# Kernel tuning notes

Hardware: AMD Instinct MI355X
Metric: run time of the kernel (lower is better)

Reference implementation:

```python
import jax, jax.numpy as jnp
import numpy as np

D_MODEL = 1024
N_HEADS = 16
D_HEAD = D_MODEL // N_HEADS
EPS_LN = 1e-5
EPS_GATE = 1e-5
EPS_DEN = 1e-5


def setup_inputs() -> dict:
    key = jax.random.key(0)
    ks = jax.random.split(key, 4)
    B, T, D = 1, 2048, D_MODEL
    x = jax.random.normal(ks[0], (B, T, D), dtype=jnp.float32)
    # Linear weights scaled like torch default init (~1/sqrt(fan_in))
    s = 1.0 / np.sqrt(D)
    qkv_w = jax.random.normal(ks[1], (3 * D, D), dtype=jnp.float32) * s
    gate_w = jax.random.normal(ks[2], (D, D), dtype=jnp.float32) * s
    proj_w = jax.random.normal(ks[3], (D, D), dtype=jnp.float32) * s
    return {
        "x": x,
        "ln_g": jnp.ones((D,), jnp.float32),
        "ln_b": jnp.zeros((D,), jnp.float32),
        "qkv_w": qkv_w,
        "qkv_b": jnp.zeros((3 * D,), jnp.float32),
        "gate_w": gate_w,
        "gate_b": jnp.zeros((D,), jnp.float32),
        "proj_w": proj_w,
        "proj_b": jnp.zeros((D,), jnp.float32),
    }


def _linear(x, w, b):
    # torch nn.Linear: y = x @ W^T + b, W is (out, in)
    return jnp.einsum("btd,od->bto", x, w) + b


def reference(x, ln_g, ln_b, qkv_w, qkv_b, gate_w, gate_b, proj_w, proj_b):
    B, T, D = x.shape
    H, Dh = N_HEADS, D_HEAD

    # LayerNorm
    mu = jnp.mean(x, axis=-1, keepdims=True)
    var = jnp.mean((x - mu) ** 2, axis=-1, keepdims=True)
    x_norm = (x - mu) / jnp.sqrt(var + EPS_LN) * ln_g + ln_b

    qkv = _linear(x_norm, qkv_w, qkv_b)
    q, k, v = jnp.split(qkv, 3, axis=-1)

    # concept gate on raw x
    gate_sig = jax.nn.sigmoid(_linear(x, gate_w, gate_b))
    gate_norm = gate_sig / (jnp.mean(gate_sig, axis=-1, keepdims=True) + EPS_GATE)
    q = q * gate_norm
    k = k * gate_norm

    # (B,T,D) -> (B,H,T,Dh)
    def heads(t):
        return t.reshape(B, T, H, Dh).transpose(0, 2, 1, 3)

    q, k, v = heads(q).astype(jnp.float32), heads(k).astype(jnp.float32), heads(v).astype(jnp.float32)

    q = jax.nn.elu(q) + 1.0
    k = jax.nn.elu(k) + 1.0

    # causal linear attention via cumsum of outer products (same math as source)
    kv = jnp.einsum("bhtd,bhtm->bhtdm", k, v)        # (B,H,T,Dh,Dh)
    kv_cum = jnp.cumsum(kv, axis=2)
    out_num = jnp.einsum("bhtd,bhtdm->bhtm", q, kv_cum)
    k_cum = jnp.cumsum(k, axis=2)
    out_den = jnp.einsum("bhtd,bhtd->bht", q, k_cum)[..., None] + EPS_DEN
    out = out_num / out_den                           # (B,H,T,Dh)

    out = out.astype(x_norm.dtype).transpose(0, 2, 1, 3).reshape(B, T, D)
    return _linear(out, proj_w, proj_b)
```

## Files before the change

kernel.cpp:

```cpp
#include <hip/hip_runtime.h>
#include <hip/hip_bf16.h>
#include <math.h>

#define T_SEQ 2048
#define DM 1024
#define NH 16
#define DH 64
#define CHUNK 64
#define NCHUNK (T_SEQ / CHUNK)

typedef __hip_bfloat16 bf16;
typedef __attribute__((ext_vector_type(8))) short short8;
typedef __attribute__((ext_vector_type(4))) short short4v;
typedef __attribute__((ext_vector_type(4))) float f32x4;

static __device__ __forceinline__ short f2b_bits(float f) {
  bf16 t = __float2bfloat16(f);
  short s;
  __builtin_memcpy(&s, &t, 2);
  return s;
}
static __device__ __forceinline__ float b2f(short s) {
  unsigned int u = ((unsigned int)(unsigned short)s) << 16;
  float f;
  __builtin_memcpy(&f, &u, 4);
  return f;
}
static __device__ __forceinline__ float gelu1(float raw, float gate, float inv) {
  float x = raw * gate * inv;
  return x > 0.f ? x + 1.f : __expf(x);
}
static __device__ __forceinline__ void gload16(const void* g, void* l) {
  __builtin_amdgcn_global_load_lds((const __attribute__((address_space(1))) void*)g,
                                   (__attribute__((address_space(3))) void*)l, 16, 0, 0);
}

#define PREP_WBLOCKS (5 * DM * DM / 4 / 256)
__global__ __launch_bounds__(256) void prep_kernel(
    const float* __restrict__ x, const float* __restrict__ g,
    const float* __restrict__ b, const float* __restrict__ qkv_w,
    const float* __restrict__ gate_w, const float* __restrict__ proj_w,
    bf16* __restrict__ xn, bf16* __restrict__ xbf,
    bf16* __restrict__ wqkv, bf16* __restrict__ wgate, bf16* __restrict__ wproj,
    float* __restrict__ gate_accum) {
  const int blk = blockIdx.x;
  if (blk < T_SEQ) {
    const int row = blk;
    if (row < 8) gate_accum[row * 256 + threadIdx.x] = 0.f;
    const float* xr = x + (size_t)row * DM;
    float vals[4];
    float s = 0.f, s2 = 0.f;
#pragma unroll
    for (int i = 0; i < 4; i++) {
      float v = xr[threadIdx.x + i * 256];
      vals[i] = v;
      s += v;
      s2 += v * v;
    }
#pragma unroll
    for (int m = 1; m < 64; m <<= 1) {
      s += __shfl_xor(s, m, 64);
      s2 += __shfl_xor(s2, m, 64);
    }
    __shared__ float red[8];
    const int wid = threadIdx.x >> 6;
    if ((threadIdx.x & 63) == 0) {
      red[wid] = s;
      red[4 + wid] = s2;
    }
    __syncthreads();
    s = red[0] + red[1] + red[2] + red[3];
    s2 = red[4] + red[5] + red[6] + red[7];
    const float mean = s * (1.f / DM);
    const float var = s2 * (1.f / DM) - mean * mean;
    const float rstd = rsqrtf(var + 1e-5f);
#pragma unroll
    for (int i = 0; i < 4; i++) {
      int idx = threadIdx.x + i * 256;
      float v = (vals[i] - mean) * rstd * g[idx] + b[idx];
      xn[(size_t)row * DM + idx] = __float2bfloat16(v);
      xbf[(size_t)row * DM + idx] = __float2bfloat16(vals[i]);
    }
  } else {
    constexpr int NQ = 3 * DM * DM / 4, NS = DM * DM / 4;
    int i = (blk - T_SEQ) * 256 + threadIdx.x;
    const float* src;
    bf16* dst;
    int j;
    if (i < NQ) { src = qkv_w; dst = wqkv; j = i; }
    else if (i < NQ + NS) { src = gate_w; dst = wgate; j = i - NQ; }
    else { src = proj_w; dst = wproj; j = i - NQ - NS; }
    float4 v = ((const float4*)src)[j];
    short4v sv;
    sv.x = f2b_bits(v.x); sv.y = f2b_bits(v.y); sv.z = f2b_bits(v.z); sv.w = f2b_bits(v.w);
    *(short4v*)&dst[j * 4] = sv;
  }
}

__global__ __launch_bounds__(256) void gemm_gateqkv(
    const bf16* __restrict__ xbf, const bf16* __restrict__ xn,
    const bf16* __restrict__ wg, const bf16* __restrict__ wq,
    const float* __restrict__ gate_b, const float* __restrict__ qkv_b,
    short* __restrict__ Gb, float* __restrict__ gate_accum,
    short* __restrict__ Qb, short* __restrict__ Kb, short* __restrict__ Vb) {
  constexpr int K = 1024;
  __shared__ __align__(16) short As[2 * 128 * 32];
  __shared__ __align__(16) short Bs[2 * 128 * 32];

  const int tid = threadIdx.x;
  const int wid = tid >> 6, lane = tid & 63;
  const int wm = wid >> 1, wn = wid & 1;
  const int lm = lane & 15, quad = lane >> 4;

  const bool isGate = blockIdx.x < 8;
  const int m0 = blockIdx.y * 128;
  const int n0 = isGate ? blockIdx.x * 128 : (blockIdx.x - 8) * 128;
  const short* Ag = (const short*)(isGate ? xbf : xn);
  const short* Wg = (const short*)(isGate ? wg : wq);

  f32x4 zero = {0.f, 0.f, 0.f, 0.f};
  f32x4 acc[4][4];
#pragma unroll
  for (int i = 0; i < 4; i++)
#pragma unroll
    for (int j = 0; j < 4; j++) acc[i][j] = zero;

  for (int kb = 0; kb < K; kb += 64) {
    __syncthreads();
#pragma unroll
    for (int sec = 0; sec < 2; sec++) {
#pragma unroll
      for (int it = 0; it < 2; it++) {
        const int idx = it * 256 + tid;
        const int row = idx >> 2, seg = (idx & 3) * 8;
        gload16(&Ag[(size_t)(m0 + row) * K + kb + sec * 32 + seg],
                &As[sec * 4096 + (it * 256 + wid * 64) * 8]);
        gload16(&Wg[(size_t)(n0 + row) * K + kb + sec * 32 + seg],
                &Bs[sec * 4096 + (it * 256 + wid * 64) * 8]);
      }
    }
    __syncthreads();
#pragma unroll
    for (int sec = 0; sec < 2; sec++) {
      short8 afr[4], bfr[4];
#pragma unroll
      for (int i = 0; i < 4; i++) {
        afr[i] = *(const short8*)&As[sec * 4096 + (wm * 64 + i * 16 + lm) * 32 + quad * 8];
        bfr[i] = *(const short8*)&Bs[sec * 4096 + (wn * 64 + i * 16 + lm) * 32 + quad * 8];
      }
#pragma unroll
      for (int i = 0; i < 4; i++)
#pragma unroll
        for (int j = 0; j < 4; j++)
          acc[i][j] = __builtin_amdgcn_mfma_f32_16x16x32_bf16(afr[i], bfr[j], acc[i][j], 0, 0, 0);
    }
  }

  if (isGate) {
    float* red = (float*)As;
    __syncthreads();
#pragma unroll
    for (int i = 0; i < 4; i++) {
#pragma unroll
      for (int r = 0; r < 4; r++) {
        const int rowl = wm * 64 + i * 16 + quad * 4 + r;
        const int row = m0 + rowl;
        float rp = 0.f;
#pragma unroll
        for (int j = 0; j < 4; j++) {
          const int col = n0 + wn * 64 + j * 16 + lm;
          float v = acc[i][j][r] + gate_b[col];
          float sig = 1.f / (1.f + __expf(-v));
          Gb[(size_t)row * DM + col] = f2b_bits(sig);
          rp += sig;
        }
        red[rowl * 32 + wn * 16 + lm] = rp;
      }
    }
    __syncthreads();
    if (tid < 128) {
      float s = 0.f;
#pragma unroll
      for (int t2 = 0; t2 < 32; t2++) s += red[tid * 32 + t2];
      atomicAdd(&gate_accum[m0 + tid], s);
    }
  } else {
#pragma unroll
    for (int i = 0; i < 4; i++) {
      const int rbase = m0 + wm * 64 + i * 16 + quad * 4;
#pragma unroll
      for (int j = 0; j < 4; j++) {
        const int col = n0 + wn * 64 + j * 16 + lm;
        const float bval = qkv_b[col];
#pragma unroll
        for (int r = 0; r < 4; r++) {
          const int row = rbase + r;
          const short bv = f2b_bits(acc[i][j][r] + bval);
          if (col < DM) {
            const int d = col;
            Qb[((size_t)(d >> 6) * T_SEQ + row) * DH + (d & 63)] = bv;
          } else if (col < 2 * DM) {
            const int d = col - DM;
            Kb[((size_t)(d >> 6) * T_SEQ + row) * DH + (d & 63)] = bv;
          } else {
            const int d = col - 2 * DM;
            Vb[((size_t)(d >> 6) * T_SEQ + row) * DH + (d & 63)] = bv;
          }
        }
      }
    }
  }
}

__global__ __launch_bounds__(256, 2) void chunk_sum_mm(const short* __restrict__ Kb,
                                                       const short* __restrict__ Gb,
                                                       const float* __restrict__ ga,
                                                       const short* __restrict__ Vb,
                                                       float* __restrict__ Skv,
                                                       float* __restrict__ Sk) {
  constexpr int STR = 68;
  __shared__ __align__(16) float Ks2[64 * STR];
  __shared__ __align__(16) float Vs2[64 * STR];
  const int b = blockIdx.x;
  const int h = b >> 5, c = b & 31;
  const int tid = threadIdx.x;
  const int ty = tid >> 4, tx = tid & 15;
  const int d0 = ty * 4, m0 = tx * 4;
  const int t0 = c * CHUNK;
  const size_t cb = ((size_t)h * T_SEQ + t0) * DH;
#pragma unroll
  for (int p = 0; p < 4; p++) {
    int f = p * 256 + tid, row = f >> 4, seg = (f & 15) * 4;
    const int t = t0 + row;
    short4v kr = *(const short4v*)&Kb[cb + row * 64 + seg];
    short4v gr = *(const short4v*)&Gb[(size_t)t * DM + h * 64 + seg];
    short4v vr = *(const short4v*)&Vb[cb + row * 64 + seg];
    const float inv = 1.f / (ga[t] * (1.f / DM) + 1e-5f);
    f32x4 kgv, vv;
#pragma unroll
    for (int e = 0; e < 4; e++) {
      kgv[e] = gelu1(b2f(kr[e]), b2f(gr[e]), inv);
      vv[e] = b2f(vr[e]);
    }
    *(f32x4*)&Ks2[row * STR + seg] = kgv;
    *(f32x4*)&Vs2[row * STR + seg] = vv;
  }
  __syncthreads();
  float acc[4][4] = {};
#pragma unroll 4
  for (int s = 0; s < 64; s++) {
    f32x4 kf = *(const f32x4*)&Ks2[s * STR + d0];
    f32x4 vf = *(const f32x4*)&Vs2[s * STR + m0];
#pragma unroll
    for (int i = 0; i < 4; i++)
#pragma unroll
      for (int j = 0; j < 4; j++) acc[i][j] += kf[i] * vf[j];
  }
  float* outp = Skv + (size_t)b * 4096;
#pragma unroll
  for (int i = 0; i < 4; i++) {
    f32x4 o = {acc[i][0], acc[i][1], acc[i][2], acc[i][3]};
    *(f32x4*)&outp[(d0 + i) * 64 + m0] = o;
  }
  if (tid < 64) {
    float ss = 0.f;
#pragma unroll 4
    for (int s = 0; s < 64; s++) ss += Ks2[s * STR + tid];
    Sk[b * 64 + tid] = ss;
  }
}

__global__ __launch_bounds__(256) void scan_excl(float* __restrict__ Skv,
                                                 float* __restrict__ Sk) {
  const int bid = blockIdx.x, tid = threadIdx.x;
  if (bid < 256) {
    const int id = bid * 256 + tid;
    const int h = id >> 12, e = id & 4095;
    float* base = Skv + (size_t)h * NCHUNK * 4096 + e;
    float v[NCHUNK];
#pragma unroll
    for (int c = 0; c < NCHUNK; c++) v[c] = base[(size_t)c * 4096];
    float run = 0.f;
#pragma unroll
    for (int c = 0; c < NCHUNK; c++) {
      float t = v[c];
      base[(size_t)c * 4096] = run;
      run += t;
    }
  } else {
    const int id = (bid - 256) * 256 + tid;
    const int h = id >> 6, e = id & 63;
    float* base = Sk + (size_t)h * NCHUNK * 64 + e;
    float v[NCHUNK];
#pragma unroll
    for (int c = 0; c < NCHUNK; c++) v[c] = base[c * 64];
    float run = 0.f;
#pragma unroll
    for (int c = 0; c < NCHUNK; c++) {
      float t = v[c];
      base[c * 64] = run;
      run += t;
    }
  }
}

__global__ __launch_bounds__(256, 2) void attn_mm(const short* __restrict__ Qb,
                                                  const short* __restrict__ Kb,
                                                  const short* __restrict__ Gb,
                                                  const float* __restrict__ ga,
                                                  const short* __restrict__ Vb,
                                                  const float* __restrict__ Skv,
                                                  const float* __restrict__ Sk,
                                                  bf16* __restrict__ O) {
  constexpr int STR = 68;
  __shared__ __align__(16) float Qs[64 * STR];
  __shared__ __align__(16) float Vs[64 * STR];
  __shared__ __align__(16) float KPs[64 * STR];
  __shared__ float denp[64 * 16];
  __shared__ float skp[64];
  __shared__ float den[64];
  const int b = blockIdx.x;
  const int h = b >> 5, c = b & 31;
  const int tid = threadIdx.x;
  const int ty = tid >> 4, tx = tid & 15;
  const int r0 = ty * 4, c0 = tx * 4, m0 = tx * 4;
  const int t0 = c * CHUNK;
  const size_t cb = ((size_t)h * T_SEQ + t0) * DH;
  const float* Pg = Skv + (size_t)b * 4096;

  short4v kreg[4], greg[4];
  float ireg[4];
#pragma unroll
  for (int q = 0; q < 4; q++) {
    int f = q * 256 + tid, row = f >> 4, seg = (f & 15) * 4;
    kreg[q] = *(const short4v*)&Kb[cb + row * 64 + seg];
    greg[q] = *(const short4v*)&Gb[(size_t)(t0 + row) * DM + h * 64 + seg];
    ireg[q] = 1.f / (ga[t0 + row] * (1.f / DM) + 1e-5f);
  }
#pragma unroll
  for (int q = 0; q < 4; q++) {
    int f = q * 256 + tid, row = f >> 4, seg = (f & 15) * 4;
    short4v qr = *(const short4v*)&Qb[cb + row * 64 + seg];
    short4v gq = *(const short4v*)&Gb[(size_t)(t0 + row) * DM + h * 64 + seg];
    short4v vr = *(const short4v*)&Vb[cb + row * 64 + seg];
    const float inv = 1.f / (ga[t0 + row] * (1.f / DM) + 1e-5f);
    f32x4 qgv, vv;
#pragma unroll
    for (int e = 0; e < 4; e++) {
      qgv[e] = gelu1(b2f(qr[e]), b2f(gq[e]), inv);
      vv[e] = b2f(vr[e]);
    }
    *(f32x4*)&Qs[row * STR + seg] = qgv;
    *(f32x4*)&Vs[row * STR + seg] = vv;
    *(f32x4*)&KPs[row * STR + seg] = *(const f32x4*)&Pg[row * 64 + seg];
  }
  if (tid < 64) skp[tid] = Sk[b * 64 + tid];
  __syncthreads();

  if (tid < 64) {
    float s = 1e-5f;
#pragma unroll 4
    for (int d = 0; d < 64; d++) s += Qs[tid * STR + d] * skp[d];
    den[tid] = s;
  }

  float accO[4][4] = {};
#pragma unroll 2
  for (int d0 = 0; d0 < 64; d0 += 4) {
    f32x4 qf[4], pf[4];
#pragma unroll
    for (int i = 0; i < 4; i++) qf[i] = *(const f32x4*)&Qs[(r0 + i) * STR + d0];
#pragma unroll
    for (int dd = 0; dd < 4; dd++) pf[dd] = *(const f32x4*)&KPs[(d0 + dd) * STR + m0];
#pragma unroll
    for (int i = 0; i < 4; i++)
#pragma unroll
      for (int j = 0; j < 4; j++)
        accO[i][j] += qf[i][0] * pf[0][j] + qf[i][1] * pf[1][j] +
                      qf[i][2] * pf[2][j] + qf[i][3] * pf[3][j];
  }
  __syncthreads();
#pragma unroll
  for (int q = 0; q < 4; q++) {
    int f = q * 256 + tid, row = f >> 4, seg = (f & 15) * 4;
    f32x4 kgv;
#pragma unroll
    for (int e = 0; e < 4; e++) kgv[e] = gelu1(b2f(kreg[q][e]), b2f(greg[q][e]), ireg[q]);
    *(f32x4*)&KPs[row * STR + seg] = kgv;
  }
  __syncthreads();

  float accS[4][4] = {};
#pragma unroll 2
  for (int d0 = 0; d0 < 64; d0 += 4) {
    f32x4 qf[4], kf[4];
#pragma unroll
    for (int i = 0; i < 4; i++) qf[i] = *(const f32x4*)&Qs[(r0 + i) * STR + d0];
#pragma unroll
    for (int j = 0; j < 4; j++) kf[j] = *(const f32x4*)&KPs[(c0 + j) * STR + d0];
#pragma unroll
    for (int i = 0; i < 4; i++)
#pragma unroll
      for (int j = 0; j < 4; j++)
        accS[i][j] += qf[i][0] * kf[j][0] + qf[i][1] * kf[j][1] +
                      qf[i][2] * kf[j][2] + qf[i][3] * kf[j][3];
  }
  float dp[4];
#pragma unroll
  for (int i = 0; i < 4; i++) {
    dp[i] = 0.f;
#pragma unroll
    for (int j = 0; j < 4; j++) {
      float v = (c0 + j) <= (r0 + i) ? accS[i][j] : 0.f;
      accS[i][j] = v;
      dp[i] += v;
    }
  }
  __syncthreads();
#pragma unroll
  for (int i = 0; i < 4; i++) {
    f32x4 sv = {accS[i][0], accS[i][1], accS[i][2], accS[i][3]};
    *(f32x4*)&Qs[(r0 + i) * STR + c0] = sv;
    denp[(r0 + i) * 16 + tx] = dp[i];
  }
  __syncthreads();
  if (tid < 64) {
    float s = den[tid];
#pragma unroll
    for (int t = 0; t < 16; t++) s += denp[tid * 16 + t];
    den[tid] = s;
  }

#pragma unroll 2
  for (int c4 = 0; c4 < 64; c4 += 4) {
    f32x4 sf[4], vf[4];
#pragma unroll
    for (int i = 0; i < 4; i++) sf[i] = *(const f32x4*)&Qs[(r0 + i) * STR + c4];
#pragma unroll
    for (int cc = 0; cc < 4; cc++) vf[cc] = *(const f32x4*)&Vs[(c4 + cc) * STR + m0];
#pragma unroll
    for (int i = 0; i < 4; i++)
#pragma unroll
      for (int j = 0; j < 4; j++)
        accO[i][j] += sf[i][0] * vf[0][j] + sf[i][1] * vf[1][j] +
                      sf[i][2] * vf[2][j] + sf[i][3] * vf[3][j];
  }
  __syncthreads();

#pragma unroll
  for (int i = 0; i < 4; i++) {
    const float inv = 1.f / den[r0 + i];
    short4v ov;
#pragma unroll
    for (int j = 0; j < 4; j++) ov[j] = f2b_bits(accO[i][j] * inv);
    *(short4v*)&O[(size_t)(t0 + r0 + i) * DM + h * 64 + m0] = ov;
  }
}

__global__ __launch_bounds__(256) void gemm_proj(const bf16* __restrict__ A,
                                                 const bf16* __restrict__ W,
                                                 const float* __restrict__ bias,
                                                 float* __restrict__ Cout) {
  constexpr int K = 1024;
  __shared__ __align__(16) short As[2 * 64 * 32];
  __shared__ __align__(16) short Bs[2 * 128 * 32];

  const int tid = threadIdx.x;
  const int wid = tid >> 6, lane = tid & 63;
  const int wm = wid >> 1, wn = wid & 1;
  const int lm = lane & 15, quad = lane >> 4;

  const int n0 = blockIdx.x * 128;
  const int m0 = blockIdx.y * 64;
  const short* Ag = (const short*)A;
  const short* Wg = (const short*)W;

  f32x4 zero = {0.f, 0.f, 0.f, 0.f};
  f32x4 acc[2][4];
#pragma unroll
  for (int i = 0; i < 2; i++)
#pragma unroll
    for (int j = 0; j < 4; j++) acc[i][j] = zero;

  for (int kb = 0; kb < K; kb += 64) {
    __syncthreads();
#pragma unroll
    for (int sec = 0; sec < 2; sec++) {
      {
        const int row = tid >> 2, seg = (tid & 3) * 8;
        gload16(&Ag[(size_t)(m0 + row) * K + kb + sec * 32 + seg],
                &As[sec * 2048 + (wid * 64) * 8]);
      }
#pragma unroll
      for (int it = 0; it < 2; it++) {
        const int idx = it * 256 + tid;
        const int row = idx >> 2, seg = (idx & 3) * 8;
        gload16(&Wg[(size_t)(n0 + row) * K + kb + sec * 32 + seg],
                &Bs[sec * 4096 + (it * 256 + wid * 64) * 8]);
      }
    }
    __syncthreads();
#pragma unroll
    for (int sec = 0; sec < 2; sec++) {
      short8 afr[2], bfr[4];
#pragma unroll
      for (int i = 0; i < 2; i++)
        afr[i] = *(const short8*)&As[sec * 2048 + (wm * 32 + i * 16 + lm) * 32 + quad * 8];
#pragma unroll
      for (int j = 0; j < 4; j++)
        bfr[j] = *(const short8*)&Bs[sec * 4096 + (wn * 64 + j * 16 + lm) * 32 + quad * 8];
#pragma unroll
      for (int i = 0; i < 2; i++)
#pragma unroll
        for (int j = 0; j < 4; j++)
          acc[i][j] = __builtin_amdgcn_mfma_f32_16x16x32_bf16(afr[i], bfr[j], acc[i][j], 0, 0, 0);
    }
  }
#pragma unroll
  for (int i = 0; i < 2; i++) {
    const int rbase = m0 + wm * 32 + i * 16 + quad * 4;
#pragma unroll
    for (int j = 0; j < 4; j++) {
      const int col = n0 + wn * 64 + j * 16 + lm;
      const float bval = bias[col];
#pragma unroll
      for (int r = 0; r < 4; r++)
        Cout[(size_t)(rbase + r) * DM + col] = acc[i][j][r] + bval;
    }
  }
}

extern "C" void kernel_launch(void* const* d_in, const int* in_sizes, int n_in,
                              void* d_out, int out_size, void* d_ws, size_t ws_size,
                              hipStream_t stream) {
  (void)in_sizes; (void)n_in; (void)out_size; (void)ws_size;
  const float* x      = (const float*)d_in[0];
  const float* ln_g   = (const float*)d_in[1];
  const float* ln_b   = (const float*)d_in[2];
  const float* qkv_w  = (const float*)d_in[3];
  const float* qkv_b  = (const float*)d_in[4];
  const float* gate_w = (const float*)d_in[5];
  const float* gate_b = (const float*)d_in[6];
  const float* proj_w = (const float*)d_in[7];
  const float* proj_b = (const float*)d_in[8];
  float* out = (float*)d_out;

  char* ws = (char*)d_ws;
  size_t off = 0;
  auto alloc = [&](size_t bytes) {
    void* p = ws + off;
    off += (bytes + 255) & ~(size_t)255;
    return p;
  };
  bf16*  xn       = (bf16*)alloc((size_t)T_SEQ * DM * 2);
  bf16*  xbf      = (bf16*)alloc((size_t)T_SEQ * DM * 2);
  bf16*  wqkv     = (bf16*)alloc((size_t)3 * DM * DM * 2);
  bf16*  wgate    = (bf16*)alloc((size_t)DM * DM * 2);
  bf16*  wproj    = (bf16*)alloc((size_t)DM * DM * 2);
  short* Gb       = (short*)alloc((size_t)T_SEQ * DM * 2);
  float* gate_accum = (float*)alloc((size_t)T_SEQ * 4);
  short* Qb       = (short*)alloc((size_t)T_SEQ * DM * 2);
  short* Kb       = (short*)alloc((size_t)T_SEQ * DM * 2);
  short* Vb       = (short*)alloc((size_t)T_SEQ * DM * 2);
  bf16*  Obuf     = (bf16*)alloc((size_t)T_SEQ * DM * 2);
  float* Skv      = (float*)alloc((size_t)NH * NCHUNK * 4096 * 4);
  float* Sk       = (float*)alloc((size_t)NH * NCHUNK * 64 * 4);

  prep_kernel<<<T_SEQ + PREP_WBLOCKS, 256, 0, stream>>>(
      x, ln_g, ln_b, qkv_w, gate_w, proj_w, xn, xbf, wqkv, wgate, wproj, gate_accum);
  gemm_gateqkv<<<dim3(32, 16), 256, 0, stream>>>(xbf, xn, wgate, wqkv, gate_b, qkv_b,
                                                 Gb, gate_accum, Qb, Kb, Vb);
  chunk_sum_mm<<<NH * NCHUNK, 256, 0, stream>>>(Kb, Gb, gate_accum, Vb, Skv, Sk);
  scan_excl<<<260, 256, 0, stream>>>(Skv, Sk);
  attn_mm<<<NH * NCHUNK, 256, 0, stream>>>(Qb, Kb, Gb, gate_accum, Vb, Skv, Sk, Obuf);
  gemm_proj<<<dim3(8, 32), 256, 0, stream>>>(Obuf, wproj, proj_b, out);
}
```

Baseline: 166.3 us.

## Rewrite chunked attention with bf16 MFMA using transposed V and state layouts

Replaces the scalar FP32 intra-chunk attention kernel with an MFMA version. Q, K, the scanned KV state and V are staged in LDS as bf16. To feed MFMA operands directly, the QKV GEMM also writes a transposed copy of V, and the chunk-sum kernel stores its KV state transposed. The QKV GEMM block index is also remapped so tiles are grouped per XCD for better L2 reuse. The costs are an extra V write, strided scalar stores in the GEMM and chunk-sum epilogues, and lower precision from rounding the state and scores to bf16.

```diff
diff --git a/kernel.cpp b/kernel.cpp
--- a/kernel.cpp
+++ b/kernel.cpp
@@ -102,7 +102,8 @@
     const bf16* __restrict__ wg, const bf16* __restrict__ wq,
     const float* __restrict__ gate_b, const float* __restrict__ qkv_b,
     short* __restrict__ Gb, float* __restrict__ gate_accum,
-    short* __restrict__ Qb, short* __restrict__ Kb, short* __restrict__ Vb) {
+    short* __restrict__ Qb, short* __restrict__ Kb, short* __restrict__ Vb,
+    short* __restrict__ VbT) {
   constexpr int K = 1024;
   __shared__ __align__(16) short As[2 * 128 * 32];
   __shared__ __align__(16) short Bs[2 * 128 * 32];
@@ -112,9 +113,15 @@
   const int wm = wid >> 1, wn = wid & 1;
   const int lm = lane & 15, quad = lane >> 4;
 
-  const bool isGate = blockIdx.x < 8;
-  const int m0 = blockIdx.y * 128;
-  const int n0 = isGate ? blockIdx.x * 128 : (blockIdx.x - 8) * 128;
+  const int bid = blockIdx.x;
+  const int xcd = bid & 7, j = bid >> 3;
+  const int mg = xcd & 1, ng = xcd >> 1;
+  const int jm = j & 7, jn = j >> 3;
+  const int mt = mg * 8 + jm;
+  const int nt = ng * 8 + jn;
+  const bool isGate = nt < 8;
+  const int m0 = mt * 128;
+  const int n0 = (isGate ? nt : nt - 8) * 128;
   const short* Ag = (const short*)(isGate ? xbf : xn);
   const short* Wg = (const short*)(isGate ? wg : wq);
 
@@ -123,7 +130,7 @@
 #pragma unroll
   for (int i = 0; i < 4; i++)
 #pragma unroll
-    for (int j = 0; j < 4; j++) acc[i][j] = zero;
+    for (int jj = 0; jj < 4; jj++) acc[i][jj] = zero;
 
   for (int kb = 0; kb < K; kb += 64) {
     __syncthreads();
@@ -151,8 +158,8 @@
 #pragma unroll
       for (int i = 0; i < 4; i++)
 #pragma unroll
-        for (int j = 0; j < 4; j++)
-          acc[i][j] = __builtin_amdgcn_mfma_f32_16x16x32_bf16(afr[i], bfr[j], acc[i][j], 0, 0, 0);
+        for (int jj = 0; jj < 4; jj++)
+          acc[i][jj] = __builtin_amdgcn_mfma_f32_16x16x32_bf16(afr[i], bfr[jj], acc[i][jj], 0, 0, 0);
     }
   }
 
@@ -167,9 +174,9 @@
         const int row = m0 + rowl;
         float rp = 0.f;
 #pragma unroll
-        for (int j = 0; j < 4; j++) {
-          const int col = n0 + wn * 64 + j * 16 + lm;
-          float v = acc[i][j][r] + gate_b[col];
+        for (int jj = 0; jj < 4; jj++) {
+          const int col = n0 + wn * 64 + jj * 16 + lm;
+          float v = acc[i][jj][r] + gate_b[col];
           float sig = 1.f / (1.f + __expf(-v));
           Gb[(size_t)row * DM + col] = f2b_bits(sig);
           rp += sig;
@@ -189,13 +196,13 @@
     for (int i = 0; i < 4; i++) {
       const int rbase = m0 + wm * 64 + i * 16 + quad * 4;
 #pragma unroll
-      for (int j = 0; j < 4; j++) {
-        const int col = n0 + wn * 64 + j * 16 + lm;
+      for (int jj = 0; jj < 4; jj++) {
+        const int col = n0 + wn * 64 + jj * 16 + lm;
         const float bval = qkv_b[col];
 #pragma unroll
         for (int r = 0; r < 4; r++) {
           const int row = rbase + r;
-          const short bv = f2b_bits(acc[i][j][r] + bval);
+          const short bv = f2b_bits(acc[i][jj][r] + bval);
           if (col < DM) {
             const int d = col;
             Qb[((size_t)(d >> 6) * T_SEQ + row) * DH + (d & 63)] = bv;
@@ -205,6 +212,7 @@
           } else {
             const int d = col - 2 * DM;
             Vb[((size_t)(d >> 6) * T_SEQ + row) * DH + (d & 63)] = bv;
+            VbT[((size_t)(d >> 6) * DH + (d & 63)) * T_SEQ + row] = bv;
           }
         }
       }
@@ -216,7 +224,7 @@
                                                        const short* __restrict__ Gb,
                                                        const float* __restrict__ ga,
                                                        const short* __restrict__ Vb,
-                                                       float* __restrict__ Skv,
+                                                       float* __restrict__ SkvT,
                                                        float* __restrict__ Sk) {
   constexpr int STR = 68;
   __shared__ __align__(16) float Ks2[64 * STR];
@@ -256,12 +264,12 @@
 #pragma unroll
       for (int j = 0; j < 4; j++) acc[i][j] += kf[i] * vf[j];
   }
-  float* outp = Skv + (size_t)b * 4096;
-#pragma unroll
-  for (int i = 0; i < 4; i++) {
-    f32x4 o = {acc[i][0], acc[i][1], acc[i][2], acc[i][3]};
-    *(f32x4*)&outp[(d0 + i) * 64 + m0] = o;
-  }
+  float* outp = SkvT + (size_t)b * 4096;
+#pragma unroll
+  for (int i = 0; i < 4; i++)
+#pragma unroll
+    for (int j = 0; j < 4; j++)
+      outp[(m0 + j) * 64 + (d0 + i)] = acc[i][j];
   if (tid < 64) {
     float ss = 0.f;
 #pragma unroll 4
@@ -304,156 +312,138 @@
   }
 }
 
-__global__ __launch_bounds__(256, 2) void attn_mm(const short* __restrict__ Qb,
-                                                  const short* __restrict__ Kb,
-                                                  const short* __restrict__ Gb,
-                                                  const float* __restrict__ ga,
-                                                  const short* __restrict__ Vb,
-                                                  const float* __restrict__ Skv,
-                                                  const float* __restrict__ Sk,
-                                                  bf16* __restrict__ O) {
-  constexpr int STR = 68;
-  __shared__ __align__(16) float Qs[64 * STR];
-  __shared__ __align__(16) float Vs[64 * STR];
-  __shared__ __align__(16) float KPs[64 * STR];
-  __shared__ float denp[64 * 16];
-  __shared__ float skp[64];
-  __shared__ float den[64];
+__global__ __launch_bounds__(256, 2) void attn_mfma(const short* __restrict__ Qb,
+                                                    const short* __restrict__ Kb,
+                                                    const short* __restrict__ Gb,
+                                                    const float* __restrict__ ga,
+                                                    const short* __restrict__ VbT,
+                                                    const float* __restrict__ SkvT,
+                                                    const float* __restrict__ Sk,
+                                                    bf16* __restrict__ O) {
+  constexpr int STR = 72;
+  __shared__ __align__(16) short Qs[64 * STR];
+  __shared__ __align__(16) short Ks[64 * STR];
+  __shared__ __align__(16) short Vt[64 * STR];
+  __shared__ __align__(16) short Pt[64 * STR];
+  __shared__ __align__(16) short SL[64 * STR];
+  __shared__ float denp[64], invden[64], skp[64];
   const int b = blockIdx.x;
   const int h = b >> 5, c = b & 31;
   const int tid = threadIdx.x;
-  const int ty = tid >> 4, tx = tid & 15;
-  const int r0 = ty * 4, c0 = tx * 4, m0 = tx * 4;
+  const int wid = tid >> 6, lane = tid & 63;
+  const int lm = lane & 15, quad = lane >> 4;
   const int t0 = c * CHUNK;
   const size_t cb = ((size_t)h * T_SEQ + t0) * DH;
-  const float* Pg = Skv + (size_t)b * 4096;
-
-  short4v kreg[4], greg[4];
-  float ireg[4];
-#pragma unroll
-  for (int q = 0; q < 4; q++) {
-    int f = q * 256 + tid, row = f >> 4, seg = (f & 15) * 4;
-    kreg[q] = *(const short4v*)&Kb[cb + row * 64 + seg];
-    greg[q] = *(const short4v*)&Gb[(size_t)(t0 + row) * DM + h * 64 + seg];
-    ireg[q] = 1.f / (ga[t0 + row] * (1.f / DM) + 1e-5f);
-  }
-#pragma unroll
-  for (int q = 0; q < 4; q++) {
-    int f = q * 256 + tid, row = f >> 4, seg = (f & 15) * 4;
+  const float* Pg = SkvT + (size_t)b * 4096;
+
+#pragma unroll
+  for (int p = 0; p < 4; p++) {
+    const int f = p * 256 + tid, row = f >> 4, seg = (f & 15) * 4;
+    const int t = t0 + row;
     short4v qr = *(const short4v*)&Qb[cb + row * 64 + seg];
-    short4v gq = *(const short4v*)&Gb[(size_t)(t0 + row) * DM + h * 64 + seg];
-    short4v vr = *(const short4v*)&Vb[cb + row * 64 + seg];
-    const float inv = 1.f / (ga[t0 + row] * (1.f / DM) + 1e-5f);
-    f32x4 qgv, vv;
+    short4v kr = *(const short4v*)&Kb[cb + row * 64 + seg];
+    short4v gr = *(const short4v*)&Gb[(size_t)t * DM + h * 64 + seg];
+    short4v vtr = *(const short4v*)&VbT[((size_t)h * DH + row) * T_SEQ + t0 + seg];
+    f32x4 pr = *(const f32x4*)&Pg[row * 64 + seg];
+    const float inv = 1.f / (ga[t] * (1.f / DM) + 1e-5f);
+    short4v qs, ks, ps;
 #pragma unroll
     for (int e = 0; e < 4; e++) {
-      qgv[e] = gelu1(b2f(qr[e]), b2f(gq[e]), inv);
-      vv[e] = b2f(vr[e]);
-    }
-    *(f32x4*)&Qs[row * STR + seg] = qgv;
-    *(f32x4*)&Vs[row * STR + seg] = vv;
-    *(f32x4*)&KPs[row * STR + seg] = *(const f32x4*)&Pg[row * 64 + seg];
+      qs[e] = f2b_bits(gelu1(b2f(qr[e]), b2f(gr[e]), inv));
+      ks[e] = f2b_bits(gelu1(b2f(kr[e]), b2f(gr[e]), inv));
+      ps[e] = f2b_bits(pr[e]);
+    }
+    *(short4v*)&Qs[row * STR + seg] = qs;
+    *(short4v*)&Ks[row * STR + seg] = ks;
+    *(short4v*)&Vt[row * STR + seg] = vtr;
+    *(short4v*)&Pt[row * STR + seg] = ps;
   }
   if (tid < 64) skp[tid] = Sk[b * 64 + tid];
   __syncthreads();
 
+  f32x4 zero = {0.f, 0.f, 0.f, 0.f};
+  short8 aq[2];
+#pragma unroll
+  for (int ks = 0; ks < 2; ks++)
+    aq[ks] = *(const short8*)&Qs[(wid * 16 + lm) * STR + ks * 32 + quad * 8];
+  f32x4 accs[4];
+#pragma unroll
+  for (int j = 0; j < 4; j++) accs[j] = zero;
+#pragma unroll
+  for (int j = 0; j < 4; j++)
+#pragma unroll
+    for (int ks = 0; ks < 2; ks++) {
+      short8 bk = *(const short8*)&Ks[(j * 16 + lm) * STR + ks * 32 + quad * 8];
+      accs[j] = __builtin_amdgcn_mfma_f32_16x16x32_bf16(aq[ks], bk, accs[j], 0, 0, 0);
+    }
+  float rowpart[4] = {0.f, 0.f, 0.f, 0.f};
+#pragma unroll
+  for (int j = 0; j < 4; j++) {
+    const int s = j * 16 + lm;
+#pragma unroll
+    for (int r = 0; r < 4; r++) {
+      const int t = wid * 16 + quad * 4 + r;
+      float v = (s <= t) ? accs[j][r] : 0.f;
+      accs[j][r] = v;
+      rowpart[r] += v;
+    }
+  }
+#pragma unroll
+  for (int msk = 1; msk < 16; msk <<= 1)
+#pragma unroll
+    for (int r = 0; r < 4; r++) rowpart[r] += __shfl_xor(rowpart[r], msk, 64);
+  if (lm == 0)
+#pragma unroll
+    for (int r = 0; r < 4; r++) denp[wid * 16 + quad * 4 + r] = rowpart[r];
+#pragma unroll
+  for (int j = 0; j < 4; j++)
+#pragma unroll
+    for (int r = 0; r < 4; r++)
+      SL[(wid * 16 + quad * 4 + r) * STR + j * 16 + lm] = f2b_bits(accs[j][r]);
+
+  f32x4 acco[4];
+#pragma unroll
+  for (int j = 0; j < 4; j++) acco[j] = zero;
+  short8 ap[2];
+#pragma unroll
+  for (int ks = 0; ks < 2; ks++)
+    ap[ks] = *(const short8*)&Pt[(wid * 16 + lm) * STR + ks * 32 + quad * 8];
+#pragma unroll
+  for (int j = 0; j < 4; j++)
+#pragma unroll
+    for (int ks = 0; ks < 2; ks++) {
+      short8 bq = *(const short8*)&Qs[(j * 16 + lm) * STR + ks * 32 + quad * 8];
+      acco[j] = __builtin_amdgcn_mfma_f32_16x16x32_bf16(ap[ks], bq, acco[j], 0, 0, 0);
+    }
+  __syncthreads();
+
   if (tid < 64) {
-    float s = 1e-5f;
-#pragma unroll 4
-    for (int d = 0; d < 64; d++) s += Qs[tid * STR + d] * skp[d];
-    den[tid] = s;
-  }
-
-  float accO[4][4] = {};
-#pragma unroll 2
-  for (int d0 = 0; d0 < 64; d0 += 4) {
-    f32x4 qf[4], pf[4];
-#pragma unroll
-    for (int i = 0; i < 4; i++) qf[i] = *(const f32x4*)&Qs[(r0 + i) * STR + d0];
-#pragma unroll
-    for (int dd = 0; dd < 4; dd++) pf[dd] = *(const f32x4*)&KPs[(d0 + dd) * STR + m0];
-#pragma unroll
-    for (int i = 0; i < 4; i++)
-#pragma unroll
-      for (int j = 0; j < 4; j++)
-        accO[i][j] += qf[i][0] * pf[0][j] + qf[i][1] * pf[1][j] +
-                      qf[i][2] * pf[2][j] + qf[i][3] * pf[3][j];
-  }
+    float s = 1e-5f + denp[tid];
+    for (int d = 0; d < 64; d++) s += b2f(Qs[tid * STR + d]) * skp[d];
+    invden[tid] = 1.f / s;
+  }
+
+  short8 av[2];
+#pragma unroll
+  for (int ks = 0; ks < 2; ks++)
+    av[ks] = *(const short8*)&Vt[(wid * 16 + lm) * STR + ks * 32 + quad * 8];
+#pragma unroll
+  for (int j = 0; j < 4; j++)
+#pragma unroll
+    for (int ks = 0; ks < 2; ks++) {
+      short8 bs = *(const short8*)&SL[(j * 16 + lm) * STR + ks * 32 + quad * 8];
+      acco[j] = __builtin_amdgcn_mfma_f32_16x16x32_bf16(av[ks], bs, acco[j], 0, 0, 0);
+    }
   __syncthreads();
-#pragma unroll
-  for (int q = 0; q < 4; q++) {
-    int f = q * 256 + tid, row = f >> 4, seg = (f & 15) * 4;
-    f32x4 kgv;
-#pragma unroll
-    for (int e = 0; e < 4; e++) kgv[e] = gelu1(b2f(kreg[q][e]), b2f(greg[q][e]), ireg[q]);
-    *(f32x4*)&KPs[row * STR + seg] = kgv;
-  }
-  __syncthreads();
-
-  float accS[4][4] = {};
-#pragma unroll 2
-  for (int d0 = 0; d0 < 64; d0 += 4) {
-    f32x4 qf[4], kf[4];
-#pragma unroll
-    for (int i = 0; i < 4; i++) qf[i] = *(const f32x4*)&Qs[(r0 + i) * STR + d0];
-#pragma unroll
-    for (int j = 0; j < 4; j++) kf[j] = *(const f32x4*)&KPs[(c0 + j) * STR + d0];
-#pragma unroll
-    for (int i = 0; i < 4; i++)
-#pragma unroll
-      for (int j = 0; j < 4; j++)
-        accS[i][j] += qf[i][0] * kf[j][0] + qf[i][1] * kf[j][1] +
-                      qf[i][2] * kf[j][2] + qf[i][3] * kf[j][3];
-  }
-  float dp[4];
-#pragma unroll
-  for (int i = 0; i < 4; i++) {
-    dp[i] = 0.f;
-#pragma unroll
-    for (int j = 0; j < 4; j++) {
-      float v = (c0 + j) <= (r0 + i) ? accS[i][j] : 0.f;
-      accS[i][j] = v;
-      dp[i] += v;
-    }
-  }
-  __syncthreads();
-#pragma unroll
-  for (int i = 0; i < 4; i++) {
-    f32x4 sv = {accS[i][0], accS[i][1], accS[i][2], accS[i][3]};
-    *(f32x4*)&Qs[(r0 + i) * STR + c0] = sv;
-    denp[(r0 + i) * 16 + tx] = dp[i];
-  }
-  __syncthreads();
-  if (tid < 64) {
-    float s = den[tid];
-#pragma unroll
-    for (int t = 0; t < 16; t++) s += denp[tid * 16 + t];
-    den[tid] = s;
-  }
-
-#pragma unroll 2
-  for (int c4 = 0; c4 < 64; c4 += 4) {
-    f32x4 sf[4], vf[4];
-#pragma unroll
-    for (int i = 0; i < 4; i++) sf[i] = *(const f32x4*)&Qs[(r0 + i) * STR + c4];
-#pragma unroll
-    for (int cc = 0; cc < 4; cc++) vf[cc] = *(const f32x4*)&Vs[(c4 + cc) * STR + m0];
-#pragma unroll
-    for (int i = 0; i < 4; i++)
-#pragma unroll
-      for (int j = 0; j < 4; j++)
-        accO[i][j] += sf[i][0] * vf[0][j] + sf[i][1] * vf[1][j] +
-                      sf[i][2] * vf[2][j] + sf[i][3] * vf[3][j];
-  }
-  __syncthreads();
-
-#pragma unroll
-  for (int i = 0; i < 4; i++) {
-    const float inv = 1.f / den[r0 + i];
+
+#pragma unroll
+  for (int j = 0; j < 4; j++) {
+    const int t = j * 16 + lm;
+    const float idv = invden[t];
     short4v ov;
 #pragma unroll
-    for (int j = 0; j < 4; j++) ov[j] = f2b_bits(accO[i][j] * inv);
-    *(short4v*)&O[(size_t)(t0 + r0 + i) * DM + h * 64 + m0] = ov;
+    for (int r = 0; r < 4; r++) ov[r] = f2b_bits(acco[j][r] * idv);
+    *(short4v*)&((short*)O)[(size_t)(t0 + t) * DM + h * 64 + wid * 16 + quad * 4] = ov;
   }
 }
 
@@ -562,16 +552,17 @@
   short* Qb       = (short*)alloc((size_t)T_SEQ * DM * 2);
   short* Kb       = (short*)alloc((size_t)T_SEQ * DM * 2);
   short* Vb       = (short*)alloc((size_t)T_SEQ * DM * 2);
+  short* VbT      = (short*)alloc((size_t)T_SEQ * DM * 2);
   bf16*  Obuf     = (bf16*)alloc((size_t)T_SEQ * DM * 2);
-  float* Skv      = (float*)alloc((size_t)NH * NCHUNK * 4096 * 4);
+  float* SkvT     = (float*)alloc((size_t)NH * NCHUNK * 4096 * 4);
   float* Sk       = (float*)alloc((size_t)NH * NCHUNK * 64 * 4);
 
   prep_kernel<<<T_SEQ + PREP_WBLOCKS, 256, 0, stream>>>(
       x, ln_g, ln_b, qkv_w, gate_w, proj_w, xn, xbf, wqkv, wgate, wproj, gate_accum);
-  gemm_gateqkv<<<dim3(32, 16), 256, 0, stream>>>(xbf, xn, wgate, wqkv, gate_b, qkv_b,
-                                                 Gb, gate_accum, Qb, Kb, Vb);
-  chunk_sum_mm<<<NH * NCHUNK, 256, 0, stream>>>(Kb, Gb, gate_accum, Vb, Skv, Sk);
-  scan_excl<<<260, 256, 0, stream>>>(Skv, Sk);
-  attn_mm<<<NH * NCHUNK, 256, 0, stream>>>(Qb, Kb, Gb, gate_accum, Vb, Skv, Sk, Obuf);
+  gemm_gateqkv<<<512, 256, 0, stream>>>(xbf, xn, wgate, wqkv, gate_b, qkv_b,
+                                        Gb, gate_accum, Qb, Kb, Vb, VbT);
+  chunk_sum_mm<<<NH * NCHUNK, 256, 0, stream>>>(Kb, Gb, gate_accum, Vb, SkvT, Sk);
+  scan_excl<<<260, 256, 0, stream>>>(SkvT, Sk);
+  attn_mfma<<<NH * NCHUNK, 256, 0, stream>>>(Qb, Kb, Gb, gate_accum, VbT, SkvT, Sk, Obuf);
   gemm_proj<<<dim3(8, 32), 256, 0, stream>>>(Obuf, wproj, proj_b, out);
 }
```

Measured after the change: 165.5 us. No clear change (-0.5%).
